# Optimization experiments

Measured on AMD Instinct MI355X. Metric: run time of the kernel, lower is better.

The kernel has to match this reference:

```python
import jax, jax.numpy as jnp
import numpy as np

LEAKY_SLOPE = 0.2

def setup_inputs() -> dict:
    key = jax.random.key(0)
    k1, k2, k3, k4, k5 = jax.random.split(key, 5)
    N, F_IN, H, D = 8192, 256, 4, 64
    x = jax.random.normal(k1, (N, F_IN), dtype=jnp.float32)
    adj = jax.random.randint(k2, (N, N), 0, 2, dtype=jnp.int32)
    W = jax.random.normal(k3, (F_IN, H * D), dtype=jnp.float32) * 0.05
    a_l = jax.random.normal(k4, (H, D), dtype=jnp.float32) * 0.05
    a_r = jax.random.normal(k5, (H, D), dtype=jnp.float32) * 0.05
    return {"x": x, "adj": adj, "W": W, "a_l": a_l, "a_r": a_r}

def reference(x, adj, W, a_l, a_r):
    N = x.shape[0]
    H, D = a_l.shape
    # projected node features: (N, H, D)
    h = (x @ W).reshape(N, H, D)
    score_l = jnp.einsum('nhd,hd->nh', h, a_l)  # (N, H)
    score_r = jnp.einsum('nhd,hd->nh', h, a_r)  # (N, H)
    # logits[i, j, h] = score_l[i, h] + score_r[j, h]
    logits = score_l[:, None, :] + score_r[None, :, :]
    logits = jax.nn.leaky_relu(logits, negative_slope=LEAKY_SLOPE)
    # mask: keep edge (i,j) if adj[i,j] + eye[i,j] != 0
    keep = (adj + jnp.eye(N, dtype=adj.dtype)) != 0  # (N, N)
    logits = jnp.where(keep[:, :, None], logits, -jnp.inf)
    # softmax over neighbors j (axis=1), matching torch softmax(dim=1)
    attn = jax.nn.softmax(logits, axis=1)  # (N, N, H)
    out = jnp.einsum('ijh,jhf->ihf', attn, h)  # (N, H, D)
    return out.reshape(N, H * D)  # concat=True
```

## Files before the change

kernel.cpp:

```cpp
#include <hip/hip_runtime.h>
#include <hip/hip_bf16.h>
#include <hip/hip_fp16.h>

#define N 8192
#define FIN 256
#define HD 256
#define LEAKY 0.2f

typedef short sh8 __attribute__((ext_vector_type(8)));
typedef _Float16 h8 __attribute__((ext_vector_type(8)));
typedef _Float16 h2 __attribute__((ext_vector_type(2)));
typedef float f32x4 __attribute__((ext_vector_type(4)));
typedef int   i32x4 __attribute__((ext_vector_type(4)));

__device__ __forceinline__ int pack2bf(float a, float b){
  __hip_bfloat162 t = __float22bfloat162_rn(make_float2(a, b));
  union { __hip_bfloat162 h; int i; } u;
  u.h = t;
  return u.i;
}

__device__ __forceinline__ h2 u2h2(unsigned u){ union{unsigned u; h2 h;} c; c.u=u; return c.h; }
__device__ __forceinline__ unsigned h22u(h2 h){ union{unsigned u; h2 h;} c; c.h=h; return c.u; }

__global__ void k_wt(const float* __restrict__ W, __hip_bfloat16* __restrict__ Wt){
  __shared__ float t[16][17];
  int tx = threadIdx.x, ty = threadIdx.y;
  int bx = blockIdx.x*16, by = blockIdx.y*16;
  t[ty][tx] = W[(by+ty)*HD + (bx+tx)];
  __syncthreads();
  Wt[(bx+ty)*FIN + (by+tx)] = __float2bfloat16(t[tx][ty]);
}

__global__ __launch_bounds__(256, 2) void k_h(
    const float* __restrict__ x, const __hip_bfloat16* __restrict__ Wt,
    const float* __restrict__ a_l, const float* __restrict__ a_r,
    _Float16* __restrict__ ht, float* __restrict__ El, float* __restrict__ El2,
    _Float16* __restrict__ Erh, _Float16* __restrict__ Er2h)
{
  const int lane = threadIdx.x & 63;
  const int w = threadIdx.x >> 6;
  const int r0 = lane & 15, q = lane >> 4;
  const int c0 = w*64;
  const int n0 = blockIdx.x*32;

  f32x4 acc[4][2];
  #pragma unroll
  for (int m = 0; m < 4; ++m)
    #pragma unroll
    for (int nt = 0; nt < 2; ++nt)
      acc[m][nt] = (f32x4){0.f, 0.f, 0.f, 0.f};

  for (int kb = 0; kb < 8; ++kb){
    const int k = kb*32 + q*8;
    sh8 af[4];
    #pragma unroll
    for (int m = 0; m < 4; ++m)
      af[m] = *(const sh8*)(Wt + (c0 + m*16 + r0)*FIN + k);
    #pragma unroll
    for (int nt = 0; nt < 2; ++nt){
      const float* xp = x + (n0 + nt*16 + r0)*FIN + k;
      f32x4 xl = *(const f32x4*)xp;
      f32x4 xh = *(const f32x4*)(xp + 4);
      union { sh8 s; int i[4]; } bx;
      bx.i[0] = pack2bf(xl[0], xl[1]);
      bx.i[1] = pack2bf(xl[2], xl[3]);
      bx.i[2] = pack2bf(xh[0], xh[1]);
      bx.i[3] = pack2bf(xh[2], xh[3]);
      #pragma unroll
      for (int m = 0; m < 4; ++m)
        acc[m][nt] = __builtin_amdgcn_mfma_f32_16x16x32_bf16(af[m], bx.s, acc[m][nt], 0, 0, 0);
    }
  }

  float pl[2] = {0.f, 0.f}, pr[2] = {0.f, 0.f};
  #pragma unroll
  for (int m = 0; m < 4; ++m){
    #pragma unroll
    for (int reg = 0; reg < 4; ++reg){
      const int c = c0 + m*16 + q*4 + reg;
      const float alv = a_l[c], arv = a_r[c];
      #pragma unroll
      for (int nt = 0; nt < 2; ++nt){
        float v = acc[m][nt][reg];
        ht[(size_t)c*N + (n0 + nt*16 + r0)] = (_Float16)v;
        pl[nt] += v*alv;
        pr[nt] += v*arv;
      }
    }
  }
  #pragma unroll
  for (int nt = 0; nt < 2; ++nt){
    pl[nt] += __shfl_xor(pl[nt], 16); pl[nt] += __shfl_xor(pl[nt], 32);
    pr[nt] += __shfl_xor(pr[nt], 16); pr[nt] += __shfl_xor(pr[nt], 32);
  }
  if (lane < 16){
    #pragma unroll
    for (int nt = 0; nt < 2; ++nt){
      const int n = n0 + nt*16 + r0;
      const float l = pl[nt], r = pr[nt];
      El  [w*N + n] = __expf(l);
      El2 [w*N + n] = __expf(LEAKY*l);
      Erh [w*N + n] = (_Float16)__expf(r);
      Er2h[w*N + n] = (_Float16)__expf(LEAKY*r);
    }
  }
}

__global__ __launch_bounds__(256) void k_bits(const int* __restrict__ adj,
                                              unsigned long long* __restrict__ bits)
{
  const int lane = threadIdx.x & 63;
  const int wid = (blockIdx.x*256 + threadIdx.x) >> 6;
  const int nw = (gridDim.x*256) >> 6;
  const int total = (N/64)*N;
  for (int idx = wid; idx < total; idx += nw){
    const int r = idx >> 7, c = idx & 127;
    int av = __builtin_nontemporal_load(adj + (size_t)r*N + c*64 + lane);
    unsigned long long b = __ballot(av != 0);
    if (c == (r >> 6)) b |= 1ull << (r & 63);
    if (lane == 0) bits[idx] = b;
  }
}

__device__ __forceinline__ void sub_compute(
    const char* frp, int loff, const _Float16* erq, const _Float16* er2q, int eoff,
    unsigned sw0, unsigned sw1, const h2 elh[2], const h2 el2h[2], int q,
    const h8& ones, f32x4 acc[2][4], f32x4 accz[2])
{
  h8 hf[4];
  #pragma unroll
  for (int d = 0; d < 4; ++d)
    hf[d] = *(const h8*)(frp + loff + d*1024);

  i32x4 er4  = *(const i32x4*)(erq  + eoff);
  i32x4 er24 = *(const i32x4*)(er2q + eoff);

  #pragma unroll
  for (int m = 0; m < 2; ++m){
    const unsigned sw = ((m == 0) ? sw0 : sw1) >> (q*8);
    unsigned fu[4];
    #pragma unroll
    for (int p = 0; p < 4; ++p){
      h2 w2 = __builtin_elementwise_max(elh[m]  * u2h2((unsigned)er4[p]),
                                        el2h[m] * u2h2((unsigned)er24[p]));
      unsigned wu = h22u(w2);
      const unsigned t = sw >> (2*p);
      wu = (t & 1u) ? wu : (wu & 0xFFFF0000u);
      wu = (t & 2u) ? wu : (wu & 0x0000FFFFu);
      fu[p] = wu;
    }
    union { h8 s; unsigned u[4]; } fa;
    fa.u[0]=fu[0]; fa.u[1]=fu[1]; fa.u[2]=fu[2]; fa.u[3]=fu[3];
    #pragma unroll
    for (int d = 0; d < 4; ++d)
      acc[m][d] = __builtin_amdgcn_mfma_f32_16x16x32_f16(fa.s, hf[d], acc[m][d], 0, 0, 0);
    accz[m] = __builtin_amdgcn_mfma_f32_16x16x32_f16(fa.s, ones, accz[m], 0, 0, 0);
  }
}

__global__ __launch_bounds__(256, 4) void k_attn(
    const unsigned* __restrict__ bits32, const _Float16* __restrict__ ht,
    const float* __restrict__ El, const float* __restrict__ El2,
    const _Float16* __restrict__ Erh, const _Float16* __restrict__ Er2h,
    float* __restrict__ part, float* __restrict__ zpart)
{
  __shared__ __align__(16) char smem[32768];
  const int b = blockIdx.x;
  const int h = b & 3, jq = (b >> 2) & 3, i128 = b >> 4;
  const int tid = threadIdx.x;
  const int lane = tid & 63;
  const int w = tid >> 6;
  const int r0 = lane & 15, q = lane >> 4;
  const int ib = i128*128 + w*32;
  const int jbase = jq * 2048;

  const _Float16* gp = ht + (size_t)(h*64 + w*16 + (lane >> 2))*N
                          + jbase + (((lane & 3) ^ ((lane >> 3) & 3))*8);
  char* lb = smem + w*1024;

  const char* frp = smem + r0*64 + ((q ^ ((r0 >> 1) & 3)) << 4);

  const float* el_ = El  + h*N + ib + r0;
  const float* el2_= El2 + h*N + ib + r0;
  h2 elh[2], el2h[2];
  #pragma unroll
  for (int m = 0; m < 2; ++m){
    _Float16 a = (_Float16)el_[m*16];
    _Float16 c = (_Float16)el2_[m*16];
    elh[m]  = (h2){a, a};
    el2h[m] = (h2){c, c};
  }
  const unsigned* bp0 = bits32 + (size_t)(ib + r0)*(N/32) + (jbase >> 5);
  const unsigned* bp1 = bp0 + 16*(N/32);
  const _Float16* erq  = Erh  + h*N + jbase + q*8;
  const _Float16* er2q = Er2h + h*N + jbase + q*8;

  union { h8 s; int i[4]; } onef;
  {
    int v = (r0 == 0) ? 0x3C003C00 : 0;
    onef.i[0]=v; onef.i[1]=v; onef.i[2]=v; onef.i[3]=v;
  }

  f32x4 acc[2][4];
  f32x4 accz[2];
  #pragma unroll
  for (int m = 0; m < 2; ++m){
    accz[m] = (f32x4){0.f,0.f,0.f,0.f};
    #pragma unroll
    for (int d = 0; d < 4; ++d)
      acc[m][d] = (f32x4){0.f,0.f,0.f,0.f};
  }

#define STAGE(bufoff, t) do { \
    const _Float16* _g = gp + (t)*128; \
    _Pragma("unroll") \
    for (int _s = 0; _s < 4; ++_s) \
      __builtin_amdgcn_global_load_lds( \
        (const __attribute__((address_space(1))) void*)(_g + _s*32), \
        (__attribute__((address_space(3))) void*)(lb + (bufoff) + _s*4096), 16, 0, 0); \
  } while(0)

  STAGE(0, 0);
  __syncthreads();

  for (int t = 0; t < 16; ++t){
    const int bo = (t & 1) ? 16384 : 0;
    const int bn = bo ^ 16384;
    const int tn = (t + 1) & 15;
    STAGE(bn, tn);

    i32x4 bw0 = *(const i32x4*)(bp0 + t*4);
    i32x4 bw1 = *(const i32x4*)(bp1 + t*4);
    #pragma unroll
    for (int ss = 0; ss < 4; ++ss)
      sub_compute(frp, bo + ss*4096, erq, er2q, t*128 + ss*32,
                  (unsigned)bw0[ss], (unsigned)bw1[ss],
                  elh, el2h, q, onef.s, acc, accz);

    __syncthreads();
  }

  if (r0 == 0){
    #pragma unroll
    for (int m = 0; m < 2; ++m)
      #pragma unroll
      for (int reg = 0; reg < 4; ++reg)
        zpart[(jq*4 + h)*N + ib + m*16 + q*4 + reg] = accz[m][reg];
  }

  float* pp = part + (size_t)jq*N*HD + h*64 + r0;
  #pragma unroll
  for (int m = 0; m < 2; ++m)
    #pragma unroll
    for (int d = 0; d < 4; ++d)
      #pragma unroll
      for (int reg = 0; reg < 4; ++reg)
        pp[(size_t)(ib + m*16 + q*4 + reg)*HD + d*16] = acc[m][d][reg];
#undef STAGE
}

__global__ void k_out(const float* __restrict__ part, const float* __restrict__ zpart,
                      float* __restrict__ out)
{
  const int t4 = (blockIdx.x*256 + threadIdx.x) * 4;
  const int i = t4 >> 8;
  const int h = (t4 & 255) >> 6;
  f32x4 a = *(const f32x4*)(part + t4);
  f32x4 bq = *(const f32x4*)(part + (size_t)N*HD + t4);
  f32x4 c = *(const f32x4*)(part + 2*(size_t)N*HD + t4);
  f32x4 d = *(const f32x4*)(part + 3*(size_t)N*HD + t4);
  float zz = zpart[h*N + i] + zpart[(4 + h)*N + i] + zpart[(8 + h)*N + i] + zpart[(12 + h)*N + i];
  f32x4 s = (a + bq + c + d) / zz;
  *(f32x4*)(out + t4) = s;
}

extern "C" void kernel_launch(void* const* d_in, const int* in_sizes, int n_in,
                              void* d_out, int out_size, void* d_ws, size_t ws_size,
                              hipStream_t stream) {
  const float* x   = (const float*)d_in[0];
  const int*   adj = (const int*)d_in[1];
  const float* W   = (const float*)d_in[2];
  const float* a_l = (const float*)d_in[3];
  const float* a_r = (const float*)d_in[4];
  float* out = (float*)d_out;

  char* ws = (char*)d_ws;
  __hip_bfloat16* Wt = (__hip_bfloat16*)ws;
  _Float16* ht   = (_Float16*)(ws + 131072);
  float*    El   = (float*)   (ws + 4325376);
  float*    El2  = (float*)   (ws + 4456448);
  _Float16* Erh  = (_Float16*)(ws + 4587520);
  _Float16* Er2h = (_Float16*)(ws + 4653056);
  unsigned long long* bits = (unsigned long long*)(ws + 4718592);
  float*    part = (float*)   (ws + 13107200);
  float*    zpart= (float*)   (ws + 46661632);

  k_wt  <<<dim3(16,16), dim3(16,16), 0, stream>>>(W, Wt);
  k_h   <<<256, 256, 0, stream>>>(x, Wt, a_l, a_r, ht, El, El2, Erh, Er2h);
  k_bits<<<4096, 256, 0, stream>>>(adj, bits);
  k_attn<<<1024, 256, 0, stream>>>((const unsigned*)bits, ht, El, El2, Erh, Er2h, part, zpart);
  k_out <<<N*HD/1024, 256, 0, stream>>>(part, zpart, out);
}
```

Before: 485.9 us.

## Fuse adjacency masking into attention kernel and drop bit-packing pass

Removes the separate kernel that packed the int32 adjacency matrix into bitmasks. The attention kernel now reads adjacency rows directly, prefetching them one sub-step ahead, and injects the self-loop diagonal in-register. Block indexing is reordered so the head index varies slowest, which may let the four per-head passes over adj hit in cache. The cost is reading the full int32 adjacency once per head instead of a compact bitmask, which raises global traffic if cache reuse is poor.

```diff
diff --git a/kernel.cpp b/kernel.cpp
--- a/kernel.cpp
+++ b/kernel.cpp
@@ -107,67 +107,15 @@
   }
 }
 
-__global__ __launch_bounds__(256) void k_bits(const int* __restrict__ adj,
-                                              unsigned long long* __restrict__ bits)
-{
-  const int lane = threadIdx.x & 63;
-  const int wid = (blockIdx.x*256 + threadIdx.x) >> 6;
-  const int nw = (gridDim.x*256) >> 6;
-  const int total = (N/64)*N;
-  for (int idx = wid; idx < total; idx += nw){
-    const int r = idx >> 7, c = idx & 127;
-    int av = __builtin_nontemporal_load(adj + (size_t)r*N + c*64 + lane);
-    unsigned long long b = __ballot(av != 0);
-    if (c == (r >> 6)) b |= 1ull << (r & 63);
-    if (lane == 0) bits[idx] = b;
-  }
-}
-
-__device__ __forceinline__ void sub_compute(
-    const char* frp, int loff, const _Float16* erq, const _Float16* er2q, int eoff,
-    unsigned sw0, unsigned sw1, const h2 elh[2], const h2 el2h[2], int q,
-    const h8& ones, f32x4 acc[2][4], f32x4 accz[2])
-{
-  h8 hf[4];
-  #pragma unroll
-  for (int d = 0; d < 4; ++d)
-    hf[d] = *(const h8*)(frp + loff + d*1024);
-
-  i32x4 er4  = *(const i32x4*)(erq  + eoff);
-  i32x4 er24 = *(const i32x4*)(er2q + eoff);
-
-  #pragma unroll
-  for (int m = 0; m < 2; ++m){
-    const unsigned sw = ((m == 0) ? sw0 : sw1) >> (q*8);
-    unsigned fu[4];
-    #pragma unroll
-    for (int p = 0; p < 4; ++p){
-      h2 w2 = __builtin_elementwise_max(elh[m]  * u2h2((unsigned)er4[p]),
-                                        el2h[m] * u2h2((unsigned)er24[p]));
-      unsigned wu = h22u(w2);
-      const unsigned t = sw >> (2*p);
-      wu = (t & 1u) ? wu : (wu & 0xFFFF0000u);
-      wu = (t & 2u) ? wu : (wu & 0x0000FFFFu);
-      fu[p] = wu;
-    }
-    union { h8 s; unsigned u[4]; } fa;
-    fa.u[0]=fu[0]; fa.u[1]=fu[1]; fa.u[2]=fu[2]; fa.u[3]=fu[3];
-    #pragma unroll
-    for (int d = 0; d < 4; ++d)
-      acc[m][d] = __builtin_amdgcn_mfma_f32_16x16x32_f16(fa.s, hf[d], acc[m][d], 0, 0, 0);
-    accz[m] = __builtin_amdgcn_mfma_f32_16x16x32_f16(fa.s, ones, accz[m], 0, 0, 0);
-  }
-}
-
 __global__ __launch_bounds__(256, 4) void k_attn(
-    const unsigned* __restrict__ bits32, const _Float16* __restrict__ ht,
+    const int* __restrict__ adj, const _Float16* __restrict__ ht,
     const float* __restrict__ El, const float* __restrict__ El2,
     const _Float16* __restrict__ Erh, const _Float16* __restrict__ Er2h,
     float* __restrict__ part, float* __restrict__ zpart)
 {
   __shared__ __align__(16) char smem[32768];
   const int b = blockIdx.x;
-  const int h = b & 3, jq = (b >> 2) & 3, i128 = b >> 4;
+  const int h = b >> 8, jq = (b >> 6) & 3, i128 = b & 63;
   const int tid = threadIdx.x;
   const int lane = tid & 63;
   const int w = tid >> 6;
@@ -178,7 +126,6 @@
   const _Float16* gp = ht + (size_t)(h*64 + w*16 + (lane >> 2))*N
                           + jbase + (((lane & 3) ^ ((lane >> 3) & 3))*8);
   char* lb = smem + w*1024;
-
   const char* frp = smem + r0*64 + ((q ^ ((r0 >> 1) & 3)) << 4);
 
   const float* el_ = El  + h*N + ib + r0;
@@ -191,10 +138,25 @@
     elh[m]  = (h2){a, a};
     el2h[m] = (h2){c, c};
   }
-  const unsigned* bp0 = bits32 + (size_t)(ib + r0)*(N/32) + (jbase >> 5);
-  const unsigned* bp1 = bp0 + 16*(N/32);
   const _Float16* erq  = Erh  + h*N + jbase + q*8;
   const _Float16* er2q = Er2h + h*N + jbase + q*8;
+
+  const int* ap0 = adj + (size_t)(ib + r0)*N + jbase + q*8;
+  const int* ap1 = ap0 + 16*N;
+
+  int td[2], sd[2], pd[2];
+  unsigned eyem[2];
+  bool db[2];
+  #pragma unroll
+  for (int m = 0; m < 2; ++m){
+    const int am = ib + m*16;
+    db[m] = ((am >> 11) == jq);
+    td[m] = (am >> 7) & 15;
+    sd[m] = (am >> 5) & 3;
+    const int dr = (am & 31) + r0;
+    pd[m] = (dr & 7) >> 1;
+    eyem[m] = ((dr >> 3) == q) ? ((dr & 1) ? 0x10000u : 1u) : 0u;
+  }
 
   union { h8 s; int i[4]; } onef;
   {
@@ -221,6 +183,15 @@
         (__attribute__((address_space(3))) void*)(lb + (bufoff) + _s*4096), 16, 0, 0); \
   } while(0)
 
+#define LD_ADJ(dst, off) do { \
+    dst[0][0] = *(const i32x4*)(ap0 + (off)); \
+    dst[0][1] = *(const i32x4*)(ap0 + (off) + 4); \
+    dst[1][0] = *(const i32x4*)(ap1 + (off)); \
+    dst[1][1] = *(const i32x4*)(ap1 + (off) + 4); \
+  } while(0)
+
+  i32x4 ac[2][2], an[2][2];
+  LD_ADJ(ac, 0);
   STAGE(0, 0);
   __syncthreads();
 
@@ -230,13 +201,47 @@
     const int tn = (t + 1) & 15;
     STAGE(bn, tn);
 
-    i32x4 bw0 = *(const i32x4*)(bp0 + t*4);
-    i32x4 bw1 = *(const i32x4*)(bp1 + t*4);
-    #pragma unroll
-    for (int ss = 0; ss < 4; ++ss)
-      sub_compute(frp, bo + ss*4096, erq, er2q, t*128 + ss*32,
-                  (unsigned)bw0[ss], (unsigned)bw1[ss],
-                  elh, el2h, q, onef.s, acc, accz);
+    #pragma unroll
+    for (int ss = 0; ss < 4; ++ss){
+      const int noff = (ss < 3) ? (t*128 + (ss+1)*32) : (tn*128);
+      LD_ADJ(an, noff);
+
+      i32x4 er4  = *(const i32x4*)(erq  + t*128 + ss*32);
+      i32x4 er24 = *(const i32x4*)(er2q + t*128 + ss*32);
+
+      h8 hf[4];
+      #pragma unroll
+      for (int d = 0; d < 4; ++d)
+        hf[d] = *(const h8*)(frp + bo + ss*4096 + d*1024);
+
+      #pragma unroll
+      for (int m = 0; m < 2; ++m){
+        const bool dg = db[m] && (t == td[m]) && (ss == sd[m]);
+        unsigned fu[4];
+        #pragma unroll
+        for (int p = 0; p < 4; ++p){
+          const int a0 = ac[m][p >> 1][(p & 1)*2];
+          const int a1 = ac[m][p >> 1][(p & 1)*2 + 1];
+          unsigned t32 = (unsigned)a0 | ((unsigned)a1 << 16);
+          if (dg) t32 |= (p == pd[m]) ? eyem[m] : 0u;
+          const unsigned msk = t32 * 0xFFFFu;
+          h2 w2 = __builtin_elementwise_max(elh[m]  * u2h2((unsigned)er4[p]),
+                                            el2h[m] * u2h2((unsigned)er24[p]));
+          fu[p] = h22u(w2) & msk;
+        }
+        union { h8 s; unsigned u[4]; } fa;
+        fa.u[0]=fu[0]; fa.u[1]=fu[1]; fa.u[2]=fu[2]; fa.u[3]=fu[3];
+        #pragma unroll
+        for (int d = 0; d < 4; ++d)
+          acc[m][d] = __builtin_amdgcn_mfma_f32_16x16x32_f16(fa.s, hf[d], acc[m][d], 0, 0, 0);
+        accz[m] = __builtin_amdgcn_mfma_f32_16x16x32_f16(fa.s, onef.s, accz[m], 0, 0, 0);
+      }
+
+      #pragma unroll
+      for (int m = 0; m < 2; ++m){
+        ac[m][0] = an[m][0]; ac[m][1] = an[m][1];
+      }
+    }
 
     __syncthreads();
   }
@@ -258,6 +263,7 @@
       for (int reg = 0; reg < 4; ++reg)
         pp[(size_t)(ib + m*16 + q*4 + reg)*HD + d*16] = acc[m][d][reg];
 #undef STAGE
+#undef LD_ADJ
 }
 
 __global__ void k_out(const float* __restrict__ part, const float* __restrict__ zpart,
@@ -292,13 +298,11 @@
   float*    El2  = (float*)   (ws + 4456448);
   _Float16* Erh  = (_Float16*)(ws + 4587520);
   _Float16* Er2h = (_Float16*)(ws + 4653056);
-  unsigned long long* bits = (unsigned long long*)(ws + 4718592);
-  float*    part = (float*)   (ws + 13107200);
-  float*    zpart= (float*)   (ws + 46661632);
+  float*    part = (float*)   (ws + 4718592);
+  float*    zpart= (float*)   (ws + 38273024);
 
   k_wt  <<<dim3(16,16), dim3(16,16), 0, stream>>>(W, Wt);
   k_h   <<<256, 256, 0, stream>>>(x, Wt, a_l, a_r, ht, El, El2, Erh, Er2h);
-  k_bits<<<4096, 256, 0, stream>>>(adj, bits);
-  k_attn<<<1024, 256, 0, stream>>>((const unsigned*)bits, ht, El, El2, Erh, Er2h, part, zpart);
+  k_attn<<<1024, 256, 0, stream>>>(adj, ht, El, El2, Erh, Er2h, part, zpart);
   k_out <<<N*HD/1024, 256, 0, stream>>>(part, zpart, out);
 }
```

New measurement: 477.3 us. About the same (-1.8%).

## Fuse bitmask build into projection kernel and reduce attention partials in-block

Applied to the files above, without the earlier changes.

Merges the adjacency bit-packing kernel into the projection kernel as extra blocks, so the two independent jobs share one launch. The attention kernel is restructured so each block owns 32 rows for one head, with each wave covering a quarter of the neighbours. Each wave keeps a private double-buffered LDS stage synchronised with waitcnt instead of block barriers, and the partial sums are reduced through LDS and normalised in-kernel. This removes the global partial buffers and the final combine kernel, at the cost of explicit waitcnt scheduling and one block-wide reduction at the end.

```diff
diff --git a/kernel.cpp b/kernel.cpp
--- a/kernel.cpp
+++ b/kernel.cpp
@@ -32,17 +32,34 @@
   Wt[(bx+ty)*FIN + (by+tx)] = __float2bfloat16(t[tx][ty]);
 }
 
-__global__ __launch_bounds__(256, 2) void k_h(
+__global__ __launch_bounds__(256, 2) void k_hb(
     const float* __restrict__ x, const __hip_bfloat16* __restrict__ Wt,
     const float* __restrict__ a_l, const float* __restrict__ a_r,
+    const int* __restrict__ adj,
     _Float16* __restrict__ ht, float* __restrict__ El, float* __restrict__ El2,
-    _Float16* __restrict__ Erh, _Float16* __restrict__ Er2h)
+    _Float16* __restrict__ Erh, _Float16* __restrict__ Er2h,
+    unsigned long long* __restrict__ bits)
 {
+  if (blockIdx.x < 4096){
+    const int lane = threadIdx.x & 63;
+    const int wid = (blockIdx.x*256 + threadIdx.x) >> 6;
+    const int nw = (4096*256) >> 6;
+    const int total = (N/64)*N;
+    for (int idx = wid; idx < total; idx += nw){
+      const int r = idx >> 7, c = idx & 127;
+      int av = __builtin_nontemporal_load(adj + (size_t)r*N + c*64 + lane);
+      unsigned long long b = __ballot(av != 0);
+      if (c == (r >> 6)) b |= 1ull << (r & 63);
+      if (lane == 0) bits[idx] = b;
+    }
+    return;
+  }
+
   const int lane = threadIdx.x & 63;
   const int w = threadIdx.x >> 6;
   const int r0 = lane & 15, q = lane >> 4;
   const int c0 = w*64;
-  const int n0 = blockIdx.x*32;
+  const int n0 = (blockIdx.x - 4096)*32;
 
   f32x4 acc[4][2];
   #pragma unroll
@@ -107,91 +124,36 @@
   }
 }
 
-__global__ __launch_bounds__(256) void k_bits(const int* __restrict__ adj,
-                                              unsigned long long* __restrict__ bits)
-{
-  const int lane = threadIdx.x & 63;
-  const int wid = (blockIdx.x*256 + threadIdx.x) >> 6;
-  const int nw = (gridDim.x*256) >> 6;
-  const int total = (N/64)*N;
-  for (int idx = wid; idx < total; idx += nw){
-    const int r = idx >> 7, c = idx & 127;
-    int av = __builtin_nontemporal_load(adj + (size_t)r*N + c*64 + lane);
-    unsigned long long b = __ballot(av != 0);
-    if (c == (r >> 6)) b |= 1ull << (r & 63);
-    if (lane == 0) bits[idx] = b;
-  }
-}
-
-__device__ __forceinline__ void sub_compute(
-    const char* frp, int loff, const _Float16* erq, const _Float16* er2q, int eoff,
-    unsigned sw0, unsigned sw1, const h2 elh[2], const h2 el2h[2], int q,
-    const h8& ones, f32x4 acc[2][4], f32x4 accz[2])
-{
-  h8 hf[4];
-  #pragma unroll
-  for (int d = 0; d < 4; ++d)
-    hf[d] = *(const h8*)(frp + loff + d*1024);
-
-  i32x4 er4  = *(const i32x4*)(erq  + eoff);
-  i32x4 er24 = *(const i32x4*)(er2q + eoff);
-
-  #pragma unroll
-  for (int m = 0; m < 2; ++m){
-    const unsigned sw = ((m == 0) ? sw0 : sw1) >> (q*8);
-    unsigned fu[4];
-    #pragma unroll
-    for (int p = 0; p < 4; ++p){
-      h2 w2 = __builtin_elementwise_max(elh[m]  * u2h2((unsigned)er4[p]),
-                                        el2h[m] * u2h2((unsigned)er24[p]));
-      unsigned wu = h22u(w2);
-      const unsigned t = sw >> (2*p);
-      wu = (t & 1u) ? wu : (wu & 0xFFFF0000u);
-      wu = (t & 2u) ? wu : (wu & 0x0000FFFFu);
-      fu[p] = wu;
-    }
-    union { h8 s; unsigned u[4]; } fa;
-    fa.u[0]=fu[0]; fa.u[1]=fu[1]; fa.u[2]=fu[2]; fa.u[3]=fu[3];
-    #pragma unroll
-    for (int d = 0; d < 4; ++d)
-      acc[m][d] = __builtin_amdgcn_mfma_f32_16x16x32_f16(fa.s, hf[d], acc[m][d], 0, 0, 0);
-    accz[m] = __builtin_amdgcn_mfma_f32_16x16x32_f16(fa.s, ones, accz[m], 0, 0, 0);
-  }
-}
-
 __global__ __launch_bounds__(256, 4) void k_attn(
     const unsigned* __restrict__ bits32, const _Float16* __restrict__ ht,
     const float* __restrict__ El, const float* __restrict__ El2,
     const _Float16* __restrict__ Erh, const _Float16* __restrict__ Er2h,
-    float* __restrict__ part, float* __restrict__ zpart)
+    float* __restrict__ out)
 {
-  __shared__ __align__(16) char smem[32768];
+  __shared__ __align__(16) char smem[33280];
   const int b = blockIdx.x;
-  const int h = b & 3, jq = (b >> 2) & 3, i128 = b >> 4;
+  const int h = b >> 8;
+  const int i0 = (b & 255) * 32;
   const int tid = threadIdx.x;
   const int lane = tid & 63;
   const int w = tid >> 6;
   const int r0 = lane & 15, q = lane >> 4;
-  const int ib = i128*128 + w*32;
-  const int jbase = jq * 2048;
-
-  const _Float16* gp = ht + (size_t)(h*64 + w*16 + (lane >> 2))*N
+  const int jbase = w * 2048;
+
+  const _Float16* gp = ht + (size_t)(h*64 + (lane >> 2))*N
                           + jbase + (((lane & 3) ^ ((lane >> 3) & 3))*8);
-  char* lb = smem + w*1024;
-
-  const char* frp = smem + r0*64 + ((q ^ ((r0 >> 1) & 3)) << 4);
-
-  const float* el_ = El  + h*N + ib + r0;
-  const float* el2_= El2 + h*N + ib + r0;
+  char* lb = smem + w*8192;
+  const char* frp = smem + w*8192 + r0*64 + ((q ^ ((r0 >> 1) & 3)) << 4);
+
   h2 elh[2], el2h[2];
   #pragma unroll
   for (int m = 0; m < 2; ++m){
-    _Float16 a = (_Float16)el_[m*16];
-    _Float16 c = (_Float16)el2_[m*16];
+    _Float16 a = (_Float16)El [h*N + i0 + m*16 + r0];
+    _Float16 c = (_Float16)El2[h*N + i0 + m*16 + r0];
     elh[m]  = (h2){a, a};
     el2h[m] = (h2){c, c};
   }
-  const unsigned* bp0 = bits32 + (size_t)(ib + r0)*(N/32) + (jbase >> 5);
+  const unsigned* bp0 = bits32 + (size_t)(i0 + r0)*(N/32) + w*64;
   const unsigned* bp1 = bp0 + 16*(N/32);
   const _Float16* erq  = Erh  + h*N + jbase + q*8;
   const _Float16* er2q = Er2h + h*N + jbase + q*8;
@@ -213,66 +175,93 @@
   }
 
 #define STAGE(bufoff, t) do { \
-    const _Float16* _g = gp + (t)*128; \
+    const _Float16* _g = gp + (t)*32; \
     _Pragma("unroll") \
     for (int _s = 0; _s < 4; ++_s) \
       __builtin_amdgcn_global_load_lds( \
-        (const __attribute__((address_space(1))) void*)(_g + _s*32), \
-        (__attribute__((address_space(3))) void*)(lb + (bufoff) + _s*4096), 16, 0, 0); \
+        (const __attribute__((address_space(1))) void*)(_g + _s*16*N), \
+        (__attribute__((address_space(3))) void*)(lb + (bufoff) + _s*1024), 16, 0, 0); \
   } while(0)
 
   STAGE(0, 0);
+
+  #pragma unroll 2
+  for (int t = 0; t < 64; ++t){
+    const int bo = (t & 1) ? 4096 : 0;
+    const int bn = bo ^ 4096;
+    const int tn = (t < 63) ? t + 1 : 63;
+
+    unsigned bw0 = bp0[t];
+    unsigned bw1 = bp1[t];
+    i32x4 er4  = *(const i32x4*)(erq  + t*32);
+    i32x4 er24 = *(const i32x4*)(er2q + t*32);
+    __builtin_amdgcn_sched_barrier(0);
+    STAGE(bn, tn);
+    __builtin_amdgcn_sched_barrier(0);
+    __builtin_amdgcn_s_waitcnt(0x0F74);
+    __builtin_amdgcn_sched_barrier(0);
+
+    h8 hf[4];
+    #pragma unroll
+    for (int d = 0; d < 4; ++d)
+      hf[d] = *(const h8*)(frp + bo + d*1024);
+
+    #pragma unroll
+    for (int m = 0; m < 2; ++m){
+      const unsigned sw = ((m == 0) ? bw0 : bw1) >> (q*8);
+      unsigned fu[4];
+      #pragma unroll
+      for (int p = 0; p < 4; ++p){
+        h2 w2 = __builtin_elementwise_max(elh[m]  * u2h2((unsigned)er4[p]),
+                                          el2h[m] * u2h2((unsigned)er24[p]));
+        unsigned lo = (sw >> (2*p)) & 1u;
+        unsigned hi = (sw >> (2*p+1)) & 1u;
+        unsigned msk = lo*0xFFFFu + hi*0xFFFF0000u;
+        fu[p] = h22u(w2) & msk;
+      }
+      union { h8 s; unsigned u[4]; } fa;
+      fa.u[0]=fu[0]; fa.u[1]=fu[1]; fa.u[2]=fu[2]; fa.u[3]=fu[3];
+      #pragma unroll
+      for (int d = 0; d < 4; ++d)
+        acc[m][d] = __builtin_amdgcn_mfma_f32_16x16x32_f16(fa.s, hf[d], acc[m][d], 0, 0, 0);
+      accz[m] = __builtin_amdgcn_mfma_f32_16x16x32_f16(fa.s, onef.s, accz[m], 0, 0, 0);
+    }
+  }
+#undef STAGE
+
+  __builtin_amdgcn_s_waitcnt(0x0F70);
+  __builtin_amdgcn_sched_barrier(0);
+
+  float* prg = (float*)(smem + w*8192);
+  #pragma unroll
+  for (int m = 0; m < 2; ++m)
+    #pragma unroll
+    for (int d = 0; d < 4; ++d)
+      #pragma unroll
+      for (int reg = 0; reg < 4; ++reg)
+        prg[(m*16 + q*4 + reg)*64 + d*16 + r0] = acc[m][d][reg];
+  if (r0 == 0){
+    float* zr = (float*)(smem + 32768 + w*128);
+    #pragma unroll
+    for (int m = 0; m < 2; ++m)
+      *(f32x4*)(zr + m*16 + q*4) = accz[m];
+  }
   __syncthreads();
 
-  for (int t = 0; t < 16; ++t){
-    const int bo = (t & 1) ? 16384 : 0;
-    const int bn = bo ^ 16384;
-    const int tn = (t + 1) & 15;
-    STAGE(bn, tn);
-
-    i32x4 bw0 = *(const i32x4*)(bp0 + t*4);
-    i32x4 bw1 = *(const i32x4*)(bp1 + t*4);
-    #pragma unroll
-    for (int ss = 0; ss < 4; ++ss)
-      sub_compute(frp, bo + ss*4096, erq, er2q, t*128 + ss*32,
-                  (unsigned)bw0[ss], (unsigned)bw1[ss],
-                  elh, el2h, q, onef.s, acc, accz);
-
-    __syncthreads();
-  }
-
-  if (r0 == 0){
-    #pragma unroll
-    for (int m = 0; m < 2; ++m)
-      #pragma unroll
-      for (int reg = 0; reg < 4; ++reg)
-        zpart[(jq*4 + h)*N + ib + m*16 + q*4 + reg] = accz[m][reg];
-  }
-
-  float* pp = part + (size_t)jq*N*HD + h*64 + r0;
-  #pragma unroll
-  for (int m = 0; m < 2; ++m)
-    #pragma unroll
-    for (int d = 0; d < 4; ++d)
-      #pragma unroll
-      for (int reg = 0; reg < 4; ++reg)
-        pp[(size_t)(ib + m*16 + q*4 + reg)*HD + d*16] = acc[m][d][reg];
-#undef STAGE
-}
-
-__global__ void k_out(const float* __restrict__ part, const float* __restrict__ zpart,
-                      float* __restrict__ out)
-{
-  const int t4 = (blockIdx.x*256 + threadIdx.x) * 4;
-  const int i = t4 >> 8;
-  const int h = (t4 & 255) >> 6;
-  f32x4 a = *(const f32x4*)(part + t4);
-  f32x4 bq = *(const f32x4*)(part + (size_t)N*HD + t4);
-  f32x4 c = *(const f32x4*)(part + 2*(size_t)N*HD + t4);
-  f32x4 d = *(const f32x4*)(part + 3*(size_t)N*HD + t4);
-  float zz = zpart[h*N + i] + zpart[(4 + h)*N + i] + zpart[(8 + h)*N + i] + zpart[(12 + h)*N + i];
-  f32x4 s = (a + bq + c + d) / zz;
-  *(f32x4*)(out + t4) = s;
+  const int r  = tid >> 3;
+  const int c8 = (tid & 7) * 8;
+  f32x4 s0 = (f32x4){0.f,0.f,0.f,0.f}, s1 = (f32x4){0.f,0.f,0.f,0.f};
+  float zz = 0.f;
+  #pragma unroll
+  for (int w4 = 0; w4 < 4; ++w4){
+    const float* p2 = (const float*)(smem + w4*8192) + r*64 + c8;
+    s0 += *(const f32x4*)p2;
+    s1 += *(const f32x4*)(p2 + 4);
+    zz += ((const float*)(smem + 32768 + w4*128))[r];
+  }
+  float* op = out + (size_t)(i0 + r)*HD + h*64 + c8;
+  *(f32x4*)op       = s0 / zz;
+  *(f32x4*)(op + 4) = s1 / zz;
 }
 
 extern "C" void kernel_launch(void* const* d_in, const int* in_sizes, int n_in,
@@ -293,12 +282,8 @@
   _Float16* Erh  = (_Float16*)(ws + 4587520);
   _Float16* Er2h = (_Float16*)(ws + 4653056);
   unsigned long long* bits = (unsigned long long*)(ws + 4718592);
-  float*    part = (float*)   (ws + 13107200);
-  float*    zpart= (float*)   (ws + 46661632);
-
-  k_wt  <<<dim3(16,16), dim3(16,16), 0, stream>>>(W, Wt);
-  k_h   <<<256, 256, 0, stream>>>(x, Wt, a_l, a_r, ht, El, El2, Erh, Er2h);
-  k_bits<<<4096, 256, 0, stream>>>(adj, bits);
-  k_attn<<<1024, 256, 0, stream>>>((const unsigned*)bits, ht, El, El2, Erh, Er2h, part, zpart);
-  k_out <<<N*HD/1024, 256, 0, stream>>>(part, zpart, out);
-}
+
+  k_wt <<<dim3(16,16), dim3(16,16), 0, stream>>>(W, Wt);
+  k_hb <<<4352, 256, 0, stream>>>(x, Wt, a_l, a_r, adj, ht, El, El2, Erh, Er2h, bits);
+  k_attn<<<1024, 256, 0, stream>>>((const unsigned*)bits, ht, El, El2, Erh, Er2h, out);
+}
```

After: 546.5 us. 12.5% more time.
